# Performance work log

Measured on AMD Instinct MI355X. Metric: run time of the kernel, lower is better.

The kernel has to match this reference:

```python
import jax, jax.numpy as jnp
import numpy as np

DIM, H, HD = 512, 8, 64
N_BANK = 4096
EPS = 1e-5


def layernorm(x, g, b):
    m = jnp.mean(x, axis=-1, keepdims=True)
    v = jnp.mean(jnp.square(x - m), axis=-1, keepdims=True)
    return (x - m) * jax.lax.rsqrt(v + EPS) * g + b


def setup_inputs() -> dict:
    key = jax.random.key(0)
    ks = jax.random.split(key, 8)
    # xavier_uniform bound for square (512,512) linears
    bound = float(np.sqrt(6.0 / (DIM + DIM)))
    inp = {
        "x_q": jax.random.normal(ks[0], (32, 128, DIM), jnp.float32),
        "x_k": jax.random.normal(ks[1], (N_BANK, DIM), jnp.float32),
        "x_v": jax.random.normal(ks[2], (N_BANK, DIM), jnp.float32),
        "Wq": jax.random.uniform(ks[3], (DIM, DIM), jnp.float32, -bound, bound),
        "Wk": jax.random.uniform(ks[4], (DIM, DIM), jnp.float32, -bound, bound),
        "Wv": jax.random.uniform(ks[5], (DIM, DIM), jnp.float32, -bound, bound),
        "Wproj": jax.random.uniform(ks[6], (DIM, DIM), jnp.float32, -bound, bound),
        "qn_g": jnp.ones((HD,), jnp.float32),
        "qn_b": jnp.zeros((HD,), jnp.float32),
        "kn_g": jnp.ones((HD,), jnp.float32),
        "kn_b": jnp.zeros((HD,), jnp.float32),
        "n_g": jnp.ones((DIM,), jnp.float32),
        "n_b": jnp.zeros((DIM,), jnp.float32),
    }
    return inp


def reference(x_q, x_k, x_v, Wq, Wk, Wv, Wproj, qn_g, qn_b, kn_g, kn_b, n_g, n_b):
    B, S, D = x_q.shape
    N = x_k.shape[0]
    scale = HD ** (-0.5)
    # Linear layers (torch: y = x @ W.T)
    q = jnp.einsum('bsd,od->bso', x_q, Wq).reshape(B, S, H, HD).transpose(0, 2, 1, 3)  # (B,H,S,hd)
    k = jnp.einsum('nd,od->no', x_k, Wk).reshape(N, H, HD).transpose(1, 0, 2)          # (H,N,hd)
    v = jnp.einsum('nd,od->no', x_v, Wv).reshape(N, H, HD).transpose(1, 0, 2)          # (H,N,hd)
    # per-head qk layernorm
    q = layernorm(q, qn_g, qn_b) * scale
    k = layernorm(k, kn_g, kn_b)
    # cross-attention to shared bank (K/V have no batch dim)
    attn = jnp.einsum('bhsd,hnd->bhsn', q, k)          # (B,H,S,N)
    attn = jax.nn.softmax(attn, axis=-1)
    x = jnp.einsum('bhsn,hnd->bhsd', attn, v)          # (B,H,S,hd)
    x = x.transpose(0, 2, 1, 3).reshape(B, S, D)
    x = layernorm(x, n_g, n_b)
    x = jnp.einsum('bsd,od->bso', x, Wproj)
    return x
```

## Files before the change

kernel.cpp:

```cpp
#include <hip/hip_runtime.h>
#include <hip/hip_bf16.h>
#include <math.h>

#define DIM 512
#define NHEAD 8
#define HD 64
#define NBANK 4096
#define NQROWS 4096
#define EPS 1e-5f
#define QSCALE 0.125f
#define PART_ELEMS (NQROWS * DIM)

typedef __attribute__((ext_vector_type(4))) float floatx4;
typedef __attribute__((ext_vector_type(8))) short short8;

__device__ __forceinline__ unsigned short f2bf(float f) {
    unsigned int u = __float_as_uint(f);
    u += 0x7fffu + ((u >> 16) & 1u);
    return (unsigned short)(u >> 16);
}
__device__ __forceinline__ float bf2f(unsigned short h) {
    return __uint_as_float(((unsigned int)h) << 16);
}
__device__ __forceinline__ unsigned int pk2(float a, float b) {
    union { __hip_bfloat162 h; unsigned int u; } cvt;
    cvt.h = __float22bfloat162_rn(make_float2(a, b));
    return cvt.u;
}

__global__ __launch_bounds__(256) void wcvt_kernel(
    const float* __restrict__ Wq, const float* __restrict__ Wk,
    const float* __restrict__ Wv, const float* __restrict__ Wp,
    unsigned short* __restrict__ Wb)
{
    const float* src = (blockIdx.y == 0) ? Wq : (blockIdx.y == 1) ? Wk
                     : (blockIdx.y == 2) ? Wv : Wp;
    unsigned short* dst = Wb + (size_t)blockIdx.y * DIM * DIM;
    const int i = (blockIdx.x * 256 + threadIdx.x) * 8;
    const float4 a0 = *(const float4*)(src + i);
    const float4 a1 = *(const float4*)(src + i + 4);
    union { short8 v; unsigned int u[4]; } t;
    t.u[0] = pk2(a0.x, a0.y); t.u[1] = pk2(a0.z, a0.w);
    t.u[2] = pk2(a1.x, a1.y); t.u[3] = pk2(a1.z, a1.w);
    *(short8*)(dst + i) = t.v;
}

__global__ __launch_bounds__(256) void qkv_kernel(
    const float* __restrict__ xq, const float* __restrict__ xk, const float* __restrict__ xv,
    const unsigned short* __restrict__ Wb,
    const float* __restrict__ qg, const float* __restrict__ qbeta,
    const float* __restrict__ kg, const float* __restrict__ kbeta,
    unsigned short* __restrict__ Qb, unsigned short* __restrict__ Kb,
    unsigned short* __restrict__ VTb)
{
    __shared__ short8 smem[1536];
    short8* as = smem;
    short8* bs = smem + 512;
    const int tid  = threadIdx.x;
    const int w    = tid >> 6, lane = tid & 63, m = lane & 15, q = lane >> 4;
    const int wr   = w & 1, wc = w >> 1;
    const int row0 = blockIdx.x * 64;
    const int mat  = blockIdx.y >> 2;
    const int col0 = (blockIdx.y & 3) * 128;
    const float* X = (mat == 0) ? xq : (mat == 1) ? xk : xv;
    const unsigned short* Wm = Wb + (size_t)mat * DIM * DIM;

    floatx4 acc[2][4];
    #pragma unroll
    for (int mt = 0; mt < 2; ++mt)
        #pragma unroll
        for (int nt = 0; nt < 4; ++nt) acc[mt][nt] = (floatx4){0.f, 0.f, 0.f, 0.f};

    for (int k0 = 0; k0 < DIM; k0 += 64) {
        #pragma unroll
        for (int p = 0; p < 6; ++p) {
            const int idx = tid + p * 256;
            if (idx < 512) {
                const int row = idx >> 3, seg = idx & 7;
                const float4* pa = (const float4*)(X + (size_t)(row0 + row) * DIM + k0 + seg * 8);
                const float4 a0 = pa[0], a1 = pa[1];
                union { short8 v; unsigned int u[4]; } ta;
                ta.u[0] = pk2(a0.x, a0.y); ta.u[1] = pk2(a0.z, a0.w);
                ta.u[2] = pk2(a1.x, a1.y); ta.u[3] = pk2(a1.z, a1.w);
                as[row * 8 + (seg ^ (row & 7))] = ta.v;
            } else {
                const int j = idx - 512;
                const int row = j >> 3, seg = j & 7;
                bs[row * 8 + (seg ^ (row & 7))] =
                    *(const short8*)(Wm + (size_t)(col0 + row) * DIM + k0 + seg * 8);
            }
        }
        __syncthreads();
        #pragma unroll
        for (int s = 0; s < 2; ++s) {
            short8 af[2], bfr[4];
            #pragma unroll
            for (int mt = 0; mt < 2; ++mt)
                af[mt] = as[(wr * 32 + mt * 16 + m) * 8 + ((s * 4 + q) ^ (m & 7))];
            #pragma unroll
            for (int nt = 0; nt < 4; ++nt)
                bfr[nt] = bs[(wc * 64 + nt * 16 + m) * 8 + ((s * 4 + q) ^ (m & 7))];
            #pragma unroll
            for (int mt = 0; mt < 2; ++mt)
                #pragma unroll
                for (int nt = 0; nt < 4; ++nt)
                    acc[mt][nt] = __builtin_amdgcn_mfma_f32_16x16x32_bf16(af[mt], bfr[nt], acc[mt][nt], 0, 0, 0);
        }
        __syncthreads();
    }

    if (mat < 2) {
        const float* g = (mat == 0) ? qg : kg;
        const float* be = (mat == 0) ? qbeta : kbeta;
        unsigned short* Y = (mat == 0) ? Qb : Kb;
        float gv[4], bv[4];
        #pragma unroll
        for (int nt = 0; nt < 4; ++nt) { gv[nt] = g[nt * 16 + m]; bv[nt] = be[nt * 16 + m]; }
        #pragma unroll
        for (int mt = 0; mt < 2; ++mt) {
            #pragma unroll
            for (int r = 0; r < 4; ++r) {
                float s = 0.f, sq = 0.f;
                #pragma unroll
                for (int nt = 0; nt < 4; ++nt) { const float v = acc[mt][nt][r]; s += v; sq += v * v; }
                s  += __shfl_xor(s, 1);  s  += __shfl_xor(s, 2);  s  += __shfl_xor(s, 4);  s  += __shfl_xor(s, 8);
                sq += __shfl_xor(sq, 1); sq += __shfl_xor(sq, 2); sq += __shfl_xor(sq, 4); sq += __shfl_xor(sq, 8);
                const float mean = s * (1.f / HD);
                const float var  = sq * (1.f / HD) - mean * mean;
                const float rr   = rsqrtf(var + EPS);
                const int grow = row0 + wr * 32 + mt * 16 + q * 4 + r;
                #pragma unroll
                for (int nt = 0; nt < 4; ++nt) {
                    float v = (acc[mt][nt][r] - mean) * rr * gv[nt] + bv[nt];
                    if (mat == 0) v *= QSCALE;
                    Y[(size_t)grow * DIM + col0 + wc * 64 + nt * 16 + m] = f2bf(v);
                }
            }
        }
    } else {
        unsigned short* vt = (unsigned short*)smem;
        #pragma unroll
        for (int mt = 0; mt < 2; ++mt)
            #pragma unroll
            for (int nt = 0; nt < 4; ++nt) {
                const int c  = wc * 64 + nt * 16 + m;
                const int rw = wr * 32 + mt * 16 + q * 4;
                *(unsigned int*)(vt + c * 88 + rw)     = pk2(acc[mt][nt][0], acc[mt][nt][1]);
                *(unsigned int*)(vt + c * 88 + rw + 2) = pk2(acc[mt][nt][2], acc[mt][nt][3]);
            }
        __syncthreads();
        #pragma unroll
        for (int p = 0; p < 4; ++p) {
            const int idx = tid + p * 256;
            const int c = idx >> 3, sg = idx & 7;
            *(short8*)(VTb + (size_t)(col0 + c) * NBANK + row0 + sg * 8) =
                *(const short8*)(vt + c * 88 + sg * 8);
        }
    }
}

__global__ __launch_bounds__(256) void attn_kernel(
    const unsigned short* __restrict__ Qb, const unsigned short* __restrict__ Kb,
    const unsigned short* __restrict__ VTb, unsigned short* __restrict__ AOp,
    float* __restrict__ sums)
{
    __shared__ short8 smem[1024];
    short8* ks  = smem;
    short8* vts = smem + 512;
    const int tid  = threadIdx.x;
    const int w    = tid >> 6;
    const int lane = tid & 63;
    const int m    = lane & 15;
    const int Qd   = lane >> 4;
    const int h    = blockIdx.x & 7;
    const int qgi  = blockIdx.x >> 3;
    const int row0 = qgi * 128;
    const int part = blockIdx.y;
    const int base0 = part * 1024;

    const int sn0 = tid >> 3,        sseg = tid & 7;
    const int sn1 = (tid + 256) >> 3;
    const unsigned short* kp0 = Kb + (size_t)sn0 * DIM + h * HD + sseg * 8;
    const unsigned short* kp1 = Kb + (size_t)sn1 * DIM + h * HD + sseg * 8;
    const unsigned short* vp0 = VTb + (size_t)(h * HD + sn0) * NBANK + (sseg >> 2) * 32 + (sseg & 3) * 4;
    const unsigned short* vp1 = VTb + (size_t)(h * HD + sn1) * NBANK + (sseg >> 2) * 32 + (sseg & 3) * 4;

    short8 qf[2][2];
    #pragma unroll
    for (int mt = 0; mt < 2; ++mt)
        #pragma unroll
        for (int s = 0; s < 2; ++s)
            qf[mt][s] = *(const short8*)(Qb + (size_t)(row0 + w * 32 + mt * 16 + m) * DIM
                                         + h * HD + s * 32 + Qd * 8);

    floatx4 of[4][2];
    float sump[2] = {0.f, 0.f};
    #pragma unroll
    for (int t = 0; t < 4; ++t)
        #pragma unroll
        for (int mt = 0; mt < 2; ++mt) of[t][mt] = (floatx4){0.f, 0.f, 0.f, 0.f};

    short8 kreg0, kreg1;
    ushort4 vlo0, vhi0, vlo1, vhi1;

    {
        kreg0 = *(const short8*)(kp0 + (size_t)base0 * DIM);
        kreg1 = *(const short8*)(kp1 + (size_t)base0 * DIM);
        vlo0 = *(const ushort4*)(vp0 + base0);  vhi0 = *(const ushort4*)(vp0 + base0 + 16);
        vlo1 = *(const ushort4*)(vp1 + base0);  vhi1 = *(const ushort4*)(vp1 + base0 + 16);
    }

    for (int c = 0; c < 16; ++c) {
        __syncthreads();
        ks[sn0 * 8 + (sseg ^ (sn0 & 7))] = kreg0;
        ks[sn1 * 8 + (sseg ^ (sn1 & 7))] = kreg1;
        {
            union { short8 v; ushort4 h4[2]; } tv;
            tv.h4[0] = vlo0; tv.h4[1] = vhi0;
            vts[sn0 * 8 + (sseg ^ (sn0 & 7))] = tv.v;
            tv.h4[0] = vlo1; tv.h4[1] = vhi1;
            vts[sn1 * 8 + (sseg ^ (sn1 & 7))] = tv.v;
        }
        __syncthreads();
        if (c < 15) {
            const int nb = base0 + (c + 1) * 64;
            kreg0 = *(const short8*)(kp0 + (size_t)nb * DIM);
            kreg1 = *(const short8*)(kp1 + (size_t)nb * DIM);
            vlo0 = *(const ushort4*)(vp0 + nb);  vhi0 = *(const ushort4*)(vp0 + nb + 16);
            vlo1 = *(const ushort4*)(vp1 + nb);  vhi1 = *(const ushort4*)(vp1 + nb + 16);
        }

        floatx4 st[4][2];
        #pragma unroll
        for (int t = 0; t < 4; ++t)
            #pragma unroll
            for (int mt = 0; mt < 2; ++mt) st[t][mt] = (floatx4){0.f, 0.f, 0.f, 0.f};
        #pragma unroll
        for (int s = 0; s < 2; ++s)
            #pragma unroll
            for (int t = 0; t < 4; ++t) {
                const short8 kf = ks[(t * 16 + m) * 8 + ((s * 4 + Qd) ^ (m & 7))];
                #pragma unroll
                for (int mt = 0; mt < 2; ++mt)
                    st[t][mt] = __builtin_amdgcn_mfma_f32_16x16x32_bf16(kf, qf[mt][s], st[t][mt], 0, 0, 0);
            }

        float p[4][2][4];
        #pragma unroll
        for (int t = 0; t < 4; ++t)
            #pragma unroll
            for (int mt = 0; mt < 2; ++mt)
                #pragma unroll
                for (int r = 0; r < 4; ++r) {
                    const float e = __expf(st[t][mt][r]);
                    p[t][mt][r] = e;
                    sump[mt] += e;
                }
        union { short8 v; unsigned int u[4]; } pf[2][2];
        #pragma unroll
        for (int mt = 0; mt < 2; ++mt)
            #pragma unroll
            for (int s2 = 0; s2 < 2; ++s2)
                #pragma unroll
                for (int u = 0; u < 4; ++u)
                    pf[mt][s2].u[u] = pk2(p[s2 * 2 + (u >> 1)][mt][(u & 1) * 2],
                                          p[s2 * 2 + (u >> 1)][mt][(u & 1) * 2 + 1]);

        #pragma unroll
        for (int s2 = 0; s2 < 2; ++s2)
            #pragma unroll
            for (int t2 = 0; t2 < 4; ++t2) {
                const short8 vf = vts[(t2 * 16 + m) * 8 + ((s2 * 4 + Qd) ^ (m & 7))];
                #pragma unroll
                for (int mt = 0; mt < 2; ++mt)
                    of[t2][mt] = __builtin_amdgcn_mfma_f32_16x16x32_bf16(vf, pf[mt][s2].v, of[t2][mt], 0, 0, 0);
            }
    }

    #pragma unroll
    for (int mt = 0; mt < 2; ++mt) {
        float s = sump[mt];
        s += __shfl_xor(s, 16);
        s += __shfl_xor(s, 32);
        sump[mt] = s;
    }
    if (Qd == 0) {
        #pragma unroll
        for (int mt = 0; mt < 2; ++mt)
            sums[((size_t)part * NQROWS + row0 + w * 32 + mt * 16 + m) * NHEAD + h] = sump[mt];
    }

    __syncthreads();
    unsigned int* ob = (unsigned int*)smem;
    #pragma unroll
    for (int t2 = 0; t2 < 4; ++t2)
        #pragma unroll
        for (int mt = 0; mt < 2; ++mt) {
            const int q  = w * 32 + mt * 16 + m;
            const int blk = t2 * 2 + (Qd >> 1);
            const int sub = (Qd & 1) * 2;
            const int bs  = (blk ^ (q & 7)) * 4;
            ob[q * 32 + bs + sub]     = pk2(of[t2][mt][0], of[t2][mt][1]);
            ob[q * 32 + bs + sub + 1] = pk2(of[t2][mt][2], of[t2][mt][3]);
        }
    __syncthreads();
    #pragma unroll
    for (int pp = 0; pp < 4; ++pp) {
        const int idx = tid + pp * 256;
        const int q = idx >> 3, sg = idx & 7;
        *(short8*)(AOp + (size_t)part * PART_ELEMS + (size_t)(row0 + q) * DIM + h * HD + sg * 8) =
            smem[q * 8 + (sg ^ (q & 7))];
    }
}

__global__ __launch_bounds__(256) void combine_kernel(
    const unsigned short* __restrict__ AOp, const float* __restrict__ sums,
    unsigned short* __restrict__ AO, float* __restrict__ meanv, float* __restrict__ rstdv)
{
    __shared__ float rs[256], rq[256];
    const int tid = threadIdx.x;
    const int row = blockIdx.x * 2 + (tid >> 7);
    const int t   = tid & 127;
    const int h   = t >> 4;

    float stot = 0.f;
    #pragma unroll
    for (int p = 0; p < 4; ++p)
        stot += sums[((size_t)p * NQROWS + row) * NHEAD + h];

    float o[4] = {0.f, 0.f, 0.f, 0.f};
    #pragma unroll
    for (int p = 0; p < 4; ++p) {
        const ushort4 u = *(const ushort4*)(AOp + (size_t)p * PART_ELEMS + (size_t)row * DIM + t * 4);
        o[0] += bf2f(u.x); o[1] += bf2f(u.y); o[2] += bf2f(u.z); o[3] += bf2f(u.w);
    }
    const float inv = 1.0f / stot;
    float v0 = o[0] * inv, v1 = o[1] * inv, v2 = o[2] * inv, v3 = o[3] * inv;

    uint2 packed;
    packed.x = pk2(v0, v1); packed.y = pk2(v2, v3);
    *(uint2*)(AO + (size_t)row * DIM + t * 4) = packed;

    rs[tid] = v0 + v1 + v2 + v3;
    rq[tid] = v0 * v0 + v1 * v1 + v2 * v2 + v3 * v3;
    __syncthreads();
    #pragma unroll
    for (int off = 64; off > 0; off >>= 1) {
        if (t < off) { rs[tid] += rs[tid + off]; rq[tid] += rq[tid + off]; }
        __syncthreads();
    }
    if (t == 0) {
        const float mean = rs[tid] * (1.f / DIM);
        const float var  = rq[tid] * (1.f / DIM) - mean * mean;
        meanv[row] = mean;
        rstdv[row] = rsqrtf(var + EPS);
    }
}

__global__ __launch_bounds__(256) void final_kernel(
    const unsigned short* __restrict__ AO, const unsigned short* __restrict__ Wpb,
    const float* __restrict__ meanv, const float* __restrict__ rstdv,
    const float* __restrict__ g, const float* __restrict__ be,
    float* __restrict__ out)
{
    __shared__ short8 fs[1024];
    __shared__ float gls[512], bls[512];
    const int tid  = threadIdx.x;
    const int w    = tid >> 6, lane = tid & 63, m = lane & 15, q = lane >> 4;
    const int row0 = blockIdx.x * 64;
    const int col0 = blockIdx.y * 64;

    #pragma unroll
    for (int i = 0; i < 2; ++i) { gls[tid + i * 256] = g[tid + i * 256]; bls[tid + i * 256] = be[tid + i * 256]; }

    floatx4 acc[4];
    #pragma unroll
    for (int mt = 0; mt < 4; ++mt) acc[mt] = (floatx4){0.f, 0.f, 0.f, 0.f};
    __syncthreads();

    for (int k0 = 0; k0 < DIM; k0 += 64) {
        #pragma unroll
        for (int p = 0; p < 4; ++p) {
            const int idx = tid + p * 256;
            if (idx < 512) {
                const int row = idx >> 3, seg = idx & 7;
                const short8 a = *(const short8*)(AO + (size_t)(row0 + row) * DIM + k0 + seg * 8);
                const float mm = meanv[row0 + row], rr = rstdv[row0 + row];
                const float* gp = gls + k0 + seg * 8;
                const float* bp = bls + k0 + seg * 8;
                float v[8];
                #pragma unroll
                for (int j = 0; j < 8; ++j)
                    v[j] = (bf2f((unsigned short)a[j]) - mm) * rr * gp[j] + bp[j];
                union { short8 s; unsigned int u[4]; } ta;
                ta.u[0] = pk2(v[0], v[1]); ta.u[1] = pk2(v[2], v[3]);
                ta.u[2] = pk2(v[4], v[5]); ta.u[3] = pk2(v[6], v[7]);
                fs[row * 8 + (seg ^ (row & 7))] = ta.s;
            } else {
                const int j = idx - 512;
                const int row = j >> 3, seg = j & 7;
                fs[512 + row * 8 + (seg ^ (row & 7))] =
                    *(const short8*)(Wpb + (size_t)(col0 + row) * DIM + k0 + seg * 8);
            }
        }
        __syncthreads();
        #pragma unroll
        for (int s = 0; s < 2; ++s) {
            short8 af[4];
            #pragma unroll
            for (int mt = 0; mt < 4; ++mt)
                af[mt] = fs[(mt * 16 + m) * 8 + ((s * 4 + q) ^ (m & 7))];
            const short8 bfr = fs[512 + (w * 16 + m) * 8 + ((s * 4 + q) ^ (m & 7))];
            #pragma unroll
            for (int mt = 0; mt < 4; ++mt)
                acc[mt] = __builtin_amdgcn_mfma_f32_16x16x32_bf16(af[mt], bfr, acc[mt], 0, 0, 0);
        }
        __syncthreads();
    }

    #pragma unroll
    for (int mt = 0; mt < 4; ++mt)
        #pragma unroll
        for (int r = 0; r < 4; ++r)
            out[(size_t)(row0 + mt * 16 + q * 4 + r) * DIM + col0 + w * 16 + m] = acc[mt][r];
}

extern "C" void kernel_launch(void* const* d_in, const int* in_sizes, int n_in,
                              void* d_out, int out_size, void* d_ws, size_t ws_size,
                              hipStream_t stream)
{
    const float* x_q = (const float*)d_in[0];
    const float* x_k = (const float*)d_in[1];
    const float* x_v = (const float*)d_in[2];
    const float* Wq  = (const float*)d_in[3];
    const float* Wk  = (const float*)d_in[4];
    const float* Wv  = (const float*)d_in[5];
    const float* Wp  = (const float*)d_in[6];
    const float* qg  = (const float*)d_in[7];
    const float* qb  = (const float*)d_in[8];
    const float* kg  = (const float*)d_in[9];
    const float* kb  = (const float*)d_in[10];
    const float* ng  = (const float*)d_in[11];
    const float* nb  = (const float*)d_in[12];
    float* out = (float*)d_out;

    unsigned short* Qb   = (unsigned short*)d_ws;
    unsigned short* Kb   = Qb  + (size_t)NQROWS * DIM;
    unsigned short* VTb  = Kb  + (size_t)NBANK * DIM;
    unsigned short* AOp  = VTb + (size_t)NBANK * DIM;
    float*          sums = (float*)(AOp + (size_t)4 * PART_ELEMS);
    float*          meanv = sums + (size_t)4 * NQROWS * NHEAD;
    float*          rstdv = meanv + NQROWS;
    unsigned short* Wb   = (unsigned short*)(rstdv + NQROWS);
    unsigned short* AO   = Qb;

    wcvt_kernel<<<dim3(128, 4), 256, 0, stream>>>(Wq, Wk, Wv, Wp, Wb);
    qkv_kernel<<<dim3(64, 12), 256, 0, stream>>>(x_q, x_k, x_v, Wb,
                                                 qg, qb, kg, kb, Qb, Kb, VTb);
    attn_kernel<<<dim3(256, 4), 256, 0, stream>>>(Qb, Kb, VTb, AOp, sums);
    combine_kernel<<<NQROWS / 2, 256, 0, stream>>>(AOp, sums, AO, meanv, rstdv);
    final_kernel<<<dim3(64, 8), 256, 0, stream>>>(AO, Wb + (size_t)3 * DIM * DIM,
                                                  meanv, rstdv, ng, nb, out);
}
```

Baseline: 180.1 us.

## Double-buffer LDS tiles in GEMM/attention kernels and fold output layernorm into combine

The qkv, attention and final kernels now use two LDS buffers with register prefetch two tiles ahead, so each loop iteration needs only one barrier and global loads overlap the MFMA work. The output layernorm is applied in combine_kernel, which writes normalized bf16 rows. As a result final_kernel no longer loads gamma/beta or mean/rstd and no longer normalizes per element. The cost is doubled LDS use, which may lower occupancy, plus more registers held for prefetch.

Result: faster. 171.5 us (-4.8%).

```diff
diff --git a/kernel.cpp b/kernel.cpp
--- a/kernel.cpp
+++ b/kernel.cpp
@@ -53,9 +53,7 @@
     unsigned short* __restrict__ Qb, unsigned short* __restrict__ Kb,
     unsigned short* __restrict__ VTb)
 {
-    __shared__ short8 smem[1536];
-    short8* as = smem;
-    short8* bs = smem + 512;
+    __shared__ short8 smem[3072];
     const int tid  = threadIdx.x;
     const int w    = tid >> 6, lane = tid & 63, m = lane & 15, q = lane >> 4;
     const int wr   = w & 1, wc = w >> 1;
@@ -65,32 +63,76 @@
     const float* X = (mat == 0) ? xq : (mat == 1) ? xk : xv;
     const unsigned short* Wm = Wb + (size_t)mat * DIM * DIM;
 
+    const int arow0 = tid >> 3,           aseg = tid & 7;
+    const int arow1 = (tid + 256) >> 3;
+    const float* ap0 = X + (size_t)(row0 + arow0) * DIM + aseg * 8;
+    const float* ap1 = X + (size_t)(row0 + arow1) * DIM + aseg * 8;
+    const int adst0 = arow0 * 8 + (aseg ^ (arow0 & 7));
+    const int adst1 = arow1 * 8 + (aseg ^ (arow1 & 7));
+    int brow[4], bdst[4];
+    const unsigned short* bp[4];
+    #pragma unroll
+    for (int j = 0; j < 4; ++j) {
+        const int idx = tid + j * 256;
+        brow[j] = idx >> 3; const int seg = idx & 7;
+        bp[j] = Wm + (size_t)(col0 + brow[j]) * DIM + seg * 8;
+        bdst[j] = brow[j] * 8 + (seg ^ (brow[j] & 7));
+    }
+
     floatx4 acc[2][4];
     #pragma unroll
     for (int mt = 0; mt < 2; ++mt)
         #pragma unroll
         for (int nt = 0; nt < 4; ++nt) acc[mt][nt] = (floatx4){0.f, 0.f, 0.f, 0.f};
 
-    for (int k0 = 0; k0 < DIM; k0 += 64) {
-        #pragma unroll
-        for (int p = 0; p < 6; ++p) {
-            const int idx = tid + p * 256;
-            if (idx < 512) {
-                const int row = idx >> 3, seg = idx & 7;
-                const float4* pa = (const float4*)(X + (size_t)(row0 + row) * DIM + k0 + seg * 8);
-                const float4 a0 = pa[0], a1 = pa[1];
-                union { short8 v; unsigned int u[4]; } ta;
-                ta.u[0] = pk2(a0.x, a0.y); ta.u[1] = pk2(a0.z, a0.w);
-                ta.u[2] = pk2(a1.x, a1.y); ta.u[3] = pk2(a1.z, a1.w);
-                as[row * 8 + (seg ^ (row & 7))] = ta.v;
-            } else {
-                const int j = idx - 512;
-                const int row = j >> 3, seg = j & 7;
-                bs[row * 8 + (seg ^ (row & 7))] =
-                    *(const short8*)(Wm + (size_t)(col0 + row) * DIM + k0 + seg * 8);
-            }
-        }
-        __syncthreads();
+    float4 pa[4];
+    short8 pb[4];
+
+    pa[0] = *(const float4*)(ap0);     pa[1] = *(const float4*)(ap0 + 4);
+    pa[2] = *(const float4*)(ap1);     pa[3] = *(const float4*)(ap1 + 4);
+    #pragma unroll
+    for (int j = 0; j < 4; ++j) pb[j] = *(const short8*)(bp[j]);
+    {
+        short8* as = smem; short8* bs = smem + 512;
+        union { short8 v; unsigned int u[4]; } ta;
+        ta.u[0] = pk2(pa[0].x, pa[0].y); ta.u[1] = pk2(pa[0].z, pa[0].w);
+        ta.u[2] = pk2(pa[1].x, pa[1].y); ta.u[3] = pk2(pa[1].z, pa[1].w);
+        as[adst0] = ta.v;
+        ta.u[0] = pk2(pa[2].x, pa[2].y); ta.u[1] = pk2(pa[2].z, pa[2].w);
+        ta.u[2] = pk2(pa[3].x, pa[3].y); ta.u[3] = pk2(pa[3].z, pa[3].w);
+        as[adst1] = ta.v;
+        #pragma unroll
+        for (int j = 0; j < 4; ++j) bs[bdst[j]] = pb[j];
+    }
+    pa[0] = *(const float4*)(ap0 + 64);  pa[1] = *(const float4*)(ap0 + 68);
+    pa[2] = *(const float4*)(ap1 + 64);  pa[3] = *(const float4*)(ap1 + 68);
+    #pragma unroll
+    for (int j = 0; j < 4; ++j) pb[j] = *(const short8*)(bp[j] + 64);
+    __syncthreads();
+
+    for (int kt = 0; kt < 8; ++kt) {
+        short8* as  = smem + (kt & 1) * 1536;
+        short8* bs  = as + 512;
+        short8* asn = smem + ((kt + 1) & 1) * 1536;
+        short8* bsn = asn + 512;
+        if (kt < 7) {
+            union { short8 v; unsigned int u[4]; } ta;
+            ta.u[0] = pk2(pa[0].x, pa[0].y); ta.u[1] = pk2(pa[0].z, pa[0].w);
+            ta.u[2] = pk2(pa[1].x, pa[1].y); ta.u[3] = pk2(pa[1].z, pa[1].w);
+            asn[adst0] = ta.v;
+            ta.u[0] = pk2(pa[2].x, pa[2].y); ta.u[1] = pk2(pa[2].z, pa[2].w);
+            ta.u[2] = pk2(pa[3].x, pa[3].y); ta.u[3] = pk2(pa[3].z, pa[3].w);
+            asn[adst1] = ta.v;
+            #pragma unroll
+            for (int j = 0; j < 4; ++j) bsn[bdst[j]] = pb[j];
+        }
+        if (kt < 6) {
+            const int o = (kt + 2) * 64;
+            pa[0] = *(const float4*)(ap0 + o);  pa[1] = *(const float4*)(ap0 + o + 4);
+            pa[2] = *(const float4*)(ap1 + o);  pa[3] = *(const float4*)(ap1 + o + 4);
+            #pragma unroll
+            for (int j = 0; j < 4; ++j) pb[j] = *(const short8*)(bp[j] + o);
+        }
         #pragma unroll
         for (int s = 0; s < 2; ++s) {
             short8 af[2], bfr[4];
@@ -164,9 +206,7 @@
     const unsigned short* __restrict__ VTb, unsigned short* __restrict__ AOp,
     float* __restrict__ sums)
 {
-    __shared__ short8 smem[1024];
-    short8* ks  = smem;
-    short8* vts = smem + 512;
+    __shared__ short8 smem[2048];
     const int tid  = threadIdx.x;
     const int w    = tid >> 6;
     const int lane = tid & 63;
@@ -180,6 +220,8 @@
 
     const int sn0 = tid >> 3,        sseg = tid & 7;
     const int sn1 = (tid + 256) >> 3;
+    const int kd0 = sn0 * 8 + (sseg ^ (sn0 & 7));
+    const int kd1 = sn1 * 8 + (sseg ^ (sn1 & 7));
     const unsigned short* kp0 = Kb + (size_t)sn0 * DIM + h * HD + sseg * 8;
     const unsigned short* kp1 = Kb + (size_t)sn1 * DIM + h * HD + sseg * 8;
     const unsigned short* vp0 = VTb + (size_t)(h * HD + sn0) * NBANK + (sseg >> 2) * 32 + (sseg & 3) * 4;
@@ -203,27 +245,36 @@
     short8 kreg0, kreg1;
     ushort4 vlo0, vhi0, vlo1, vhi1;
 
+    kreg0 = *(const short8*)(kp0 + (size_t)base0 * DIM);
+    kreg1 = *(const short8*)(kp1 + (size_t)base0 * DIM);
+    vlo0 = *(const ushort4*)(vp0 + base0);  vhi0 = *(const ushort4*)(vp0 + base0 + 16);
+    vlo1 = *(const ushort4*)(vp1 + base0);  vhi1 = *(const ushort4*)(vp1 + base0 + 16);
     {
-        kreg0 = *(const short8*)(kp0 + (size_t)base0 * DIM);
-        kreg1 = *(const short8*)(kp1 + (size_t)base0 * DIM);
-        vlo0 = *(const ushort4*)(vp0 + base0);  vhi0 = *(const ushort4*)(vp0 + base0 + 16);
-        vlo1 = *(const ushort4*)(vp1 + base0);  vhi1 = *(const ushort4*)(vp1 + base0 + 16);
-    }
+        short8* ks = smem; short8* vts = smem + 512;
+        ks[kd0] = kreg0; ks[kd1] = kreg1;
+        union { short8 v; ushort4 h4[2]; } tv;
+        tv.h4[0] = vlo0; tv.h4[1] = vhi0;  vts[kd0] = tv.v;
+        tv.h4[0] = vlo1; tv.h4[1] = vhi1;  vts[kd1] = tv.v;
+    }
+    kreg0 = *(const short8*)(kp0 + (size_t)(base0 + 64) * DIM);
+    kreg1 = *(const short8*)(kp1 + (size_t)(base0 + 64) * DIM);
+    vlo0 = *(const ushort4*)(vp0 + base0 + 64);  vhi0 = *(const ushort4*)(vp0 + base0 + 80);
+    vlo1 = *(const ushort4*)(vp1 + base0 + 64);  vhi1 = *(const ushort4*)(vp1 + base0 + 80);
+    __syncthreads();
 
     for (int c = 0; c < 16; ++c) {
-        __syncthreads();
-        ks[sn0 * 8 + (sseg ^ (sn0 & 7))] = kreg0;
-        ks[sn1 * 8 + (sseg ^ (sn1 & 7))] = kreg1;
-        {
+        short8* ks   = smem + (c & 1) * 1024;
+        short8* vts  = ks + 512;
+        short8* ksn  = smem + ((c + 1) & 1) * 1024;
+        short8* vtsn = ksn + 512;
+        if (c < 15) {
+            ksn[kd0] = kreg0; ksn[kd1] = kreg1;
             union { short8 v; ushort4 h4[2]; } tv;
-            tv.h4[0] = vlo0; tv.h4[1] = vhi0;
-            vts[sn0 * 8 + (sseg ^ (sn0 & 7))] = tv.v;
-            tv.h4[0] = vlo1; tv.h4[1] = vhi1;
-            vts[sn1 * 8 + (sseg ^ (sn1 & 7))] = tv.v;
-        }
-        __syncthreads();
-        if (c < 15) {
-            const int nb = base0 + (c + 1) * 64;
+            tv.h4[0] = vlo0; tv.h4[1] = vhi0;  vtsn[kd0] = tv.v;
+            tv.h4[0] = vlo1; tv.h4[1] = vhi1;  vtsn[kd1] = tv.v;
+        }
+        if (c < 14) {
+            const int nb = base0 + (c + 2) * 64;
             kreg0 = *(const short8*)(kp0 + (size_t)nb * DIM);
             kreg1 = *(const short8*)(kp1 + (size_t)nb * DIM);
             vlo0 = *(const ushort4*)(vp0 + nb);  vhi0 = *(const ushort4*)(vp0 + nb + 16);
@@ -275,6 +326,7 @@
                 for (int mt = 0; mt < 2; ++mt)
                     of[t2][mt] = __builtin_amdgcn_mfma_f32_16x16x32_bf16(vf, pf[mt][s2].v, of[t2][mt], 0, 0, 0);
             }
+        __syncthreads();
     }
 
     #pragma unroll
@@ -290,7 +342,6 @@
             sums[((size_t)part * NQROWS + row0 + w * 32 + mt * 16 + m) * NHEAD + h] = sump[mt];
     }
 
-    __syncthreads();
     unsigned int* ob = (unsigned int*)smem;
     #pragma unroll
     for (int t2 = 0; t2 < 4; ++t2)
@@ -315,13 +366,15 @@
 
 __global__ __launch_bounds__(256) void combine_kernel(
     const unsigned short* __restrict__ AOp, const float* __restrict__ sums,
-    unsigned short* __restrict__ AO, float* __restrict__ meanv, float* __restrict__ rstdv)
+    const float* __restrict__ g, const float* __restrict__ be,
+    unsigned short* __restrict__ AO)
 {
-    __shared__ float rs[256], rq[256];
-    const int tid = threadIdx.x;
-    const int row = blockIdx.x * 2 + (tid >> 7);
-    const int t   = tid & 127;
-    const int h   = t >> 4;
+    __shared__ float rs[256], rq[256], sm[2], sr[2];
+    const int tid  = threadIdx.x;
+    const int half = tid >> 7;
+    const int row  = blockIdx.x * 2 + half;
+    const int t    = tid & 127;
+    const int h    = t >> 4;
 
     float stot = 0.f;
     #pragma unroll
@@ -335,11 +388,7 @@
         o[0] += bf2f(u.x); o[1] += bf2f(u.y); o[2] += bf2f(u.z); o[3] += bf2f(u.w);
     }
     const float inv = 1.0f / stot;
-    float v0 = o[0] * inv, v1 = o[1] * inv, v2 = o[2] * inv, v3 = o[3] * inv;
-
-    uint2 packed;
-    packed.x = pk2(v0, v1); packed.y = pk2(v2, v3);
-    *(uint2*)(AO + (size_t)row * DIM + t * 4) = packed;
+    const float v0 = o[0] * inv, v1 = o[1] * inv, v2 = o[2] * inv, v3 = o[3] * inv;
 
     rs[tid] = v0 + v1 + v2 + v3;
     rq[tid] = v0 * v0 + v1 * v1 + v2 * v2 + v3 * v3;
@@ -352,65 +401,73 @@
     if (t == 0) {
         const float mean = rs[tid] * (1.f / DIM);
         const float var  = rq[tid] * (1.f / DIM) - mean * mean;
-        meanv[row] = mean;
-        rstdv[row] = rsqrtf(var + EPS);
-    }
+        sm[half] = mean;
+        sr[half] = rsqrtf(var + EPS);
+    }
+    __syncthreads();
+
+    const float mean = sm[half], rstd = sr[half];
+    const float4 g4 = *(const float4*)(g + t * 4);
+    const float4 b4 = *(const float4*)(be + t * 4);
+    uint2 packed;
+    packed.x = pk2((v0 - mean) * rstd * g4.x + b4.x, (v1 - mean) * rstd * g4.y + b4.y);
+    packed.y = pk2((v2 - mean) * rstd * g4.z + b4.z, (v3 - mean) * rstd * g4.w + b4.w);
+    *(uint2*)(AO + (size_t)row * DIM + t * 4) = packed;
 }
 
 __global__ __launch_bounds__(256) void final_kernel(
     const unsigned short* __restrict__ AO, const unsigned short* __restrict__ Wpb,
-    const float* __restrict__ meanv, const float* __restrict__ rstdv,
-    const float* __restrict__ g, const float* __restrict__ be,
     float* __restrict__ out)
 {
-    __shared__ short8 fs[1024];
-    __shared__ float gls[512], bls[512];
+    __shared__ short8 fs[2048];
     const int tid  = threadIdx.x;
     const int w    = tid >> 6, lane = tid & 63, m = lane & 15, q = lane >> 4;
     const int row0 = blockIdx.x * 64;
     const int col0 = blockIdx.y * 64;
 
-    #pragma unroll
-    for (int i = 0; i < 2; ++i) { gls[tid + i * 256] = g[tid + i * 256]; bls[tid + i * 256] = be[tid + i * 256]; }
+    const int r0 = tid >> 3,           sseg = tid & 7;
+    const int r1 = (tid + 256) >> 3;
+    const int d0 = r0 * 8 + (sseg ^ (r0 & 7));
+    const int d1 = r1 * 8 + (sseg ^ (r1 & 7));
+    const unsigned short* ap0 = AO  + (size_t)(row0 + r0) * DIM + sseg * 8;
+    const unsigned short* ap1 = AO  + (size_t)(row0 + r1) * DIM + sseg * 8;
+    const unsigned short* wp0 = Wpb + (size_t)(col0 + r0) * DIM + sseg * 8;
+    const unsigned short* wp1 = Wpb + (size_t)(col0 + r1) * DIM + sseg * 8;
 
     floatx4 acc[4];
     #pragma unroll
     for (int mt = 0; mt < 4; ++mt) acc[mt] = (floatx4){0.f, 0.f, 0.f, 0.f};
+
+    short8 pa0, pa1, pw0, pw1;
+    pa0 = *(const short8*)(ap0);       pa1 = *(const short8*)(ap1);
+    pw0 = *(const short8*)(wp0);       pw1 = *(const short8*)(wp1);
+    {
+        fs[d0] = pa0; fs[d1] = pa1;
+        fs[512 + d0] = pw0; fs[512 + d1] = pw1;
+    }
+    pa0 = *(const short8*)(ap0 + 64);  pa1 = *(const short8*)(ap1 + 64);
+    pw0 = *(const short8*)(wp0 + 64);  pw1 = *(const short8*)(wp1 + 64);
     __syncthreads();
 
-    for (int k0 = 0; k0 < DIM; k0 += 64) {
-        #pragma unroll
-        for (int p = 0; p < 4; ++p) {
-            const int idx = tid + p * 256;
-            if (idx < 512) {
-                const int row = idx >> 3, seg = idx & 7;
-                const short8 a = *(const short8*)(AO + (size_t)(row0 + row) * DIM + k0 + seg * 8);
-                const float mm = meanv[row0 + row], rr = rstdv[row0 + row];
-                const float* gp = gls + k0 + seg * 8;
-                const float* bp = bls + k0 + seg * 8;
-                float v[8];
-                #pragma unroll
-                for (int j = 0; j < 8; ++j)
-                    v[j] = (bf2f((unsigned short)a[j]) - mm) * rr * gp[j] + bp[j];
-                union { short8 s; unsigned int u[4]; } ta;
-                ta.u[0] = pk2(v[0], v[1]); ta.u[1] = pk2(v[2], v[3]);
-                ta.u[2] = pk2(v[4], v[5]); ta.u[3] = pk2(v[6], v[7]);
-                fs[row * 8 + (seg ^ (row & 7))] = ta.s;
-            } else {
-                const int j = idx - 512;
-                const int row = j >> 3, seg = j & 7;
-                fs[512 + row * 8 + (seg ^ (row & 7))] =
-                    *(const short8*)(Wpb + (size_t)(col0 + row) * DIM + k0 + seg * 8);
-            }
-        }
-        __syncthreads();
+    for (int kt = 0; kt < 8; ++kt) {
+        short8* buf  = fs + (kt & 1) * 1024;
+        short8* bufn = fs + ((kt + 1) & 1) * 1024;
+        if (kt < 7) {
+            bufn[d0] = pa0; bufn[d1] = pa1;
+            bufn[512 + d0] = pw0; bufn[512 + d1] = pw1;
+        }
+        if (kt < 6) {
+            const int o = (kt + 2) * 64;
+            pa0 = *(const short8*)(ap0 + o);  pa1 = *(const short8*)(ap1 + o);
+            pw0 = *(const short8*)(wp0 + o);  pw1 = *(const short8*)(wp1 + o);
+        }
         #pragma unroll
         for (int s = 0; s < 2; ++s) {
             short8 af[4];
             #pragma unroll
             for (int mt = 0; mt < 4; ++mt)
-                af[mt] = fs[(mt * 16 + m) * 8 + ((s * 4 + q) ^ (m & 7))];
-            const short8 bfr = fs[512 + (w * 16 + m) * 8 + ((s * 4 + q) ^ (m & 7))];
+                af[mt] = buf[(mt * 16 + m) * 8 + ((s * 4 + q) ^ (m & 7))];
+            const short8 bfr = buf[512 + (w * 16 + m) * 8 + ((s * 4 + q) ^ (m & 7))];
             #pragma unroll
             for (int mt = 0; mt < 4; ++mt)
                 acc[mt] = __builtin_amdgcn_mfma_f32_16x16x32_bf16(af[mt], bfr, acc[mt], 0, 0, 0);
@@ -449,16 +506,13 @@
     unsigned short* VTb  = Kb  + (size_t)NBANK * DIM;
     unsigned short* AOp  = VTb + (size_t)NBANK * DIM;
     float*          sums = (float*)(AOp + (size_t)4 * PART_ELEMS);
-    float*          meanv = sums + (size_t)4 * NQROWS * NHEAD;
-    float*          rstdv = meanv + NQROWS;
-    unsigned short* Wb   = (unsigned short*)(rstdv + NQROWS);
+    unsigned short* Wb   = (unsigned short*)(sums + (size_t)4 * NQROWS * NHEAD);
     unsigned short* AO   = Qb;
 
     wcvt_kernel<<<dim3(128, 4), 256, 0, stream>>>(Wq, Wk, Wv, Wp, Wb);
     qkv_kernel<<<dim3(64, 12), 256, 0, stream>>>(x_q, x_k, x_v, Wb,
                                                  qg, qb, kg, kb, Qb, Kb, VTb);
     attn_kernel<<<dim3(256, 4), 256, 0, stream>>>(Qb, Kb, VTb, AOp, sums);
-    combine_kernel<<<NQROWS / 2, 256, 0, stream>>>(AOp, sums, AO, meanv, rstdv);
-    final_kernel<<<dim3(64, 8), 256, 0, stream>>>(AO, Wb + (size_t)3 * DIM * DIM,
-                                                  meanv, rstdv, ng, nb, out);
-}
+    combine_kernel<<<NQROWS / 2, 256, 0, stream>>>(AOp, sums, ng, nb, AO);
+    final_kernel<<<dim3(64, 8), 256, 0, stream>>>(AO, Wb + (size_t)3 * DIM * DIM, out);
+}
```
